# Optimization experiments

Hardware: AMD Instinct MI355X
Metric: run time of the kernel (lower is better)

Reference implementation:

```python
import jax, jax.numpy as jnp
import numpy as np
import math

B, N, C = 256, 196, 784   # n_tokens == HW == inter_dim required by the RPE matmul
HEADS = 4
HGT, WID = 14, 14
D = C // HEADS            # 196


def setup_inputs() -> dict:
    key = jax.random.key(0)
    ks = jax.random.split(key, 11)
    s = 0.02  # typical linear init scale, keeps softmax logits sane
    return {
        "x":     jax.random.normal(ks[0], (B, N, C), jnp.float32),
        "Wq":    jax.random.normal(ks[1], (C, C), jnp.float32) * s,
        "bq":    jnp.zeros((C,), jnp.float32),
        "Wk":    jax.random.normal(ks[2], (C, C), jnp.float32) * s,
        "bk":    jnp.zeros((C,), jnp.float32),
        "Wv":    jax.random.normal(ks[3], (C, C), jnp.float32) * s,
        "bv":    jnp.zeros((C,), jnp.float32),
        "Wo":    jax.random.normal(ks[4], (C, C), jnp.float32) * s,
        "bo":    jnp.zeros((C,), jnp.float32),
        "rel_h": jax.random.normal(ks[5], (1, HEADS, D, HGT, 1), jnp.float32),
        "rel_w": jax.random.normal(ks[6], (1, HEADS, D, 1, WID), jnp.float32),
    }


def reference(x, Wq, bq, Wk, bk, Wv, bv, Wo, bo, rel_h, rel_w):
    b, n, c = x.shape
    h, d = HEADS, c // HEADS

    def split_heads(t):  # (b, n, c) -> (b, h, n, d)
        return t.reshape(b, n, h, d).transpose(0, 2, 1, 3)

    q = split_heads(x @ Wq.T + bq)
    k = split_heads(x @ Wk.T + bk)
    v = split_heads(x @ Wv.T + bv)

    # (b, h, n, n) scaled dot-product scores
    sim = jnp.einsum('bhnd,bhmd->bhnm', q, k) / math.sqrt(d)

    # RPE bias: (rel_h + rel_w) -> (h, d, HW) -> (h, HW, d); matmul with q
    # treats q's token axis as the contraction axis (faithful to source).
    cp = (rel_h + rel_w).reshape(h, d, HGT * WID).transpose(0, 2, 1)  # (h, HW, d)
    pos = jnp.einsum('hpk,bhkc->bhpc', cp, q)  # (b, h, HW, d) == (b, h, n, n)

    attn = jax.nn.softmax(sim + pos, axis=-1)
    out = jnp.einsum('bhnm,bhmd->bhnd', attn, v)      # (b, h, n, d)
    out = out.transpose(0, 2, 1, 3).reshape(b, n, c)  # (b, n, c)
    return out @ Wo.T + bo
```

## Files before the change

kernel.cpp:

```cpp
#include <hip/hip_runtime.h>
#include <hip/hip_bf16.h>
#include <stdint.h>


using bf16 = __hip_bfloat16;
typedef __bf16   bf16x8 __attribute__((ext_vector_type(8)));
typedef __bf16   bf16x4 __attribute__((ext_vector_type(4)));
typedef float    f32x4  __attribute__((ext_vector_type(4)));

#define PADN 224
#define MATE (PADN*PADN)
#define MATB2 (MATE*2)
#define WROWS 896
#define KPAD 800
#define XROWB (KPAD*2)

__device__ __forceinline__ void gload16(void* lds, const void* g) {
  __builtin_amdgcn_global_load_lds(
      (const __attribute__((address_space(1))) void*)g,
      (__attribute__((address_space(3))) void*)lds, 16, 0, 0);
}

__device__ __forceinline__ void mfma_tiles(const char* bufA, const char* bufB,
                                           f32x4 (&acc)[4][4], int wr, int wc,
                                           int lane) {
  const int q = lane >> 4, c = lane & 15;
  bf16x8 a[4], b[4];
#pragma unroll
  for (int i = 0; i < 4; ++i)
    a[i] = *(const bf16x8*)(bufA + ((wr * 64 + i * 16 + c) << 6) + (q << 4));
#pragma unroll
  for (int j = 0; j < 4; ++j)
    b[j] = *(const bf16x8*)(bufB + ((wc * 64 + j * 16 + c) << 6) + (q << 4));
#pragma unroll
  for (int i = 0; i < 4; ++i)
#pragma unroll
    for (int j = 0; j < 4; ++j)
      acc[i][j] = __builtin_amdgcn_mfma_f32_16x16x32_bf16(a[i], b[j], acc[i][j], 0, 0, 0);
}

template <int EPI>
__global__ __launch_bounds__(256) void gemm_proj(
    const bf16* __restrict__ A, const bf16* __restrict__ B,
    const float* __restrict__ bias, bf16* __restrict__ d1,
    bf16* __restrict__ d2, float* __restrict__ dF, int M) {
  __shared__ __align__(16) char smem[16384];
  char* bufA = smem;
  char* bufB = smem + 8192;
  const int tid = threadIdx.x, lane = tid & 63, wave = tid >> 6;
  const int wr = wave >> 1, wc = wave & 1;
  const int m0 = blockIdx.x * 128, n0 = blockIdx.y * 128;

  f32x4 acc[4][4] = {};

  const int r0 = wave * 32 + (lane >> 2);
  const int bo = (lane & 3) << 4;
  const char* gA = (const char*)A + (size_t)(m0 + r0) * XROWB + bo;
  const char* gB = (const char*)B + (size_t)(n0 + r0) * XROWB + bo;
  char* lA = bufA + wave * 2048;
  char* lB = bufB + wave * 2048;

  for (int kc = 0; kc < 25; ++kc) {
    const int ko = kc * 64;
    gload16(lA,        gA + ko);
    gload16(lA + 1024, gA + 16 * XROWB + ko);
    gload16(lB,        gB + ko);
    gload16(lB + 1024, gB + 16 * XROWB + ko);
    __syncthreads();
    mfma_tiles(bufA, bufB, acc, wr, wc, lane);
    __syncthreads();
  }

  const int q = lane >> 4, c = lane & 15;
  if (EPI == 0 || EPI == 1) {
#pragma unroll
    for (int j = 0; j < 4; ++j) {
      const int col = n0 + wc * 64 + j * 16 + c;
      if (col >= 784) continue;
      const float bs = bias[col];
      const int hh = col / 196, dd = col - hh * 196;
#pragma unroll
      for (int i = 0; i < 4; ++i)
#pragma unroll
        for (int r = 0; r < 4; ++r) {
          const int row = m0 + wr * 64 + i * 16 + q * 4 + r;
          const int b = row / 196, n = row - b * 196;
          d1[(size_t)(b * 4 + hh) * MATE + (size_t)n * PADN + dd] =
              __float2bfloat16(acc[i][j][r] + bs);
        }
    }
  } else if (EPI == 4) {
#pragma unroll
    for (int j = 0; j < 4; ++j) {
      const int col = n0 + wc * 64 + j * 16 + c;
      if (col >= 784) continue;
      const float bs = bias[col];
#pragma unroll
      for (int i = 0; i < 4; ++i)
#pragma unroll
        for (int r = 0; r < 4; ++r) {
          const int row = m0 + wr * 64 + i * 16 + q * 4 + r;
          dF[(size_t)row * 784 + col] = acc[i][j][r] + bs;
        }
    }
  } else {
#pragma unroll
    for (int i = 0; i < 4; ++i)
#pragma unroll
      for (int r = 0; r < 4; ++r) {
        const int row = m0 + wr * 64 + i * 16 + q * 4 + r;
        if (row >= 784) continue;
        const float bs = bias[row];
        const int hh = row / 196, dd = row - hh * 196;
#pragma unroll
        for (int j = 0; j < 4; ++j) {
          const int col = n0 + wc * 64 + j * 16 + c;
          const int b = col / 196, n = col - b * 196;
          const float v = acc[i][j][r] + bs;
          const size_t o = (size_t)(b * 4 + hh) * MATE + (size_t)dd * PADN + n;
          const bf16 hv = __float2bfloat16(v);
          d1[o] = hv;
          if (EPI == 2) d2[o] = __float2bfloat16(v - __bfloat162float(hv));
        }
      }
  }
}

__global__ __launch_bounds__(256) void attn_score(
    const bf16* __restrict__ Q, const bf16* __restrict__ K,
    const bf16* __restrict__ CPh, const bf16* __restrict__ CPl,
    const bf16* __restrict__ Qth, const bf16* __restrict__ Qtl,
    float* __restrict__ S) {
  __shared__ __align__(16) char smem[24576];
  char* bufA = smem;
  char* bufB = smem + 8192;
  char* bufC = smem + 16384;
  const int tid = threadIdx.x, lane = tid & 63, wave = tid >> 6;
  const int wr = wave >> 1, wc = wave & 1;
  const int bh = blockIdx.z, h = bh & 3;
  const int m0 = blockIdx.x * 128, n0 = blockIdx.y * 128;

  f32x4 acc[4][4] = {};

  const int r0 = wave * 32 + (lane >> 2);
  const int bo = (lane & 3) << 4;
  const size_t la = (size_t)(m0 + r0) * 448 + bo;
  const size_t lb = (size_t)(n0 + r0) * 448 + bo;
  const size_t bhB = (size_t)bh * MATB2, hB = (size_t)h * MATB2;
  const char* aQ  = (const char*)Q   + bhB + la;
  const char* aK  = (const char*)K   + bhB + lb;
  const char* aCh = (const char*)CPh + hB  + la;
  const char* aCl = (const char*)CPl + hB  + la;
  const char* aTh = (const char*)Qth + bhB + lb;
  const char* aTl = (const char*)Qtl + bhB + lb;
  char* lA = bufA + wave * 2048;
  char* lB = bufB + wave * 2048;
  char* lC = bufC + wave * 2048;

  for (int kc = 0; kc < 7; ++kc) {
    const int ko = kc * 64;
    gload16(lA, aQ + ko); gload16(lA + 1024, aQ + 16 * 448 + ko);
    gload16(lB, aK + ko); gload16(lB + 1024, aK + 16 * 448 + ko);
    __syncthreads();
    mfma_tiles(bufA, bufB, acc, wr, wc, lane);
    __syncthreads();
  }
#pragma unroll
  for (int i = 0; i < 4; ++i)
#pragma unroll
    for (int j = 0; j < 4; ++j) acc[i][j] = acc[i][j] * (1.0f / 14.0f);

  for (int kc = 0; kc < 7; ++kc) {
    const int ko = kc * 64;
    gload16(lA, aCh + ko); gload16(lA + 1024, aCh + 16 * 448 + ko);
    gload16(lB, aTh + ko); gload16(lB + 1024, aTh + 16 * 448 + ko);
    gload16(lC, aTl + ko); gload16(lC + 1024, aTl + 16 * 448 + ko);
    __syncthreads();
    mfma_tiles(bufA, bufB, acc, wr, wc, lane);
    mfma_tiles(bufA, bufC, acc, wr, wc, lane);
    __syncthreads();
  }

  for (int kc = 0; kc < 7; ++kc) {
    const int ko = kc * 64;
    gload16(lA, aCl + ko); gload16(lA + 1024, aCl + 16 * 448 + ko);
    gload16(lB, aTh + ko); gload16(lB + 1024, aTh + 16 * 448 + ko);
    __syncthreads();
    mfma_tiles(bufA, bufB, acc, wr, wc, lane);
    __syncthreads();
  }

  float* Sb = S + (size_t)bh * MATE;
  const int q = lane >> 4, c = lane & 15;
#pragma unroll
  for (int i = 0; i < 4; ++i)
#pragma unroll
    for (int j = 0; j < 4; ++j)
#pragma unroll
      for (int r = 0; r < 4; ++r) {
        const int row = m0 + wr * 64 + i * 16 + q * 4 + r;
        const int col = n0 + wc * 64 + j * 16 + c;
        if (row < 196 && col < PADN) Sb[(size_t)row * PADN + col] = acc[i][j][r];
      }
}

__global__ __launch_bounds__(256) void softmax_k(const float* __restrict__ S,
                                                 bf16* __restrict__ P) {
  const int bh = blockIdx.y;
  const int row = blockIdx.x * 4 + (threadIdx.x >> 6);
  const int lane = threadIdx.x & 63;
  bf16* Pr = P + (size_t)bh * MATE + (size_t)row * PADN;
  if (row >= 196) {
#pragma unroll
    for (int k = 0; k < 4; ++k) {
      const int m = lane + k * 64;
      if (m < PADN) Pr[m] = __float2bfloat16(0.f);
    }
    return;
  }
  const float* Sr = S + (size_t)bh * MATE + (size_t)row * PADN;
  float v[4];
  float mx = -1e30f;
#pragma unroll
  for (int k = 0; k < 4; ++k) {
    const int m = lane + k * 64;
    v[k] = (m < 196) ? Sr[m] : -1e30f;
    mx = fmaxf(mx, v[k]);
  }
#pragma unroll
  for (int off = 32; off; off >>= 1) mx = fmaxf(mx, __shfl_xor(mx, off));
  float s = 0.f;
#pragma unroll
  for (int k = 0; k < 4; ++k) {
    const int m = lane + k * 64;
    v[k] = (m < 196) ? __expf(v[k] - mx) : 0.f;
    s += v[k];
  }
#pragma unroll
  for (int off = 32; off; off >>= 1) s += __shfl_xor(s, off);
  const float inv = 1.0f / s;
#pragma unroll
  for (int k = 0; k < 4; ++k) {
    const int m = lane + k * 64;
    if (m < PADN) Pr[m] = __float2bfloat16((m < 196) ? v[k] * inv : 0.f);
  }
}

__global__ __launch_bounds__(256) void attn_pv(const bf16* __restrict__ P,
                                               const bf16* __restrict__ Vt,
                                               bf16* __restrict__ O) {
  __shared__ __align__(16) char smem[16384];
  char* bufA = smem;
  char* bufB = smem + 8192;
  const int tid = threadIdx.x, lane = tid & 63, wave = tid >> 6;
  const int wr = wave >> 1, wc = wave & 1;
  const int bh = blockIdx.z;
  const int m0 = blockIdx.x * 128, n0 = blockIdx.y * 128;

  f32x4 acc[4][4] = {};

  const int r0 = wave * 32 + (lane >> 2);
  const int bo = (lane & 3) << 4;
  const size_t bhB = (size_t)bh * MATB2;
  const char* aP = (const char*)P  + bhB + (size_t)(m0 + r0) * 448 + bo;
  const char* aV = (const char*)Vt + bhB + (size_t)(n0 + r0) * 448 + bo;
  char* lA = bufA + wave * 2048;
  char* lB = bufB + wave * 2048;

  for (int kc = 0; kc < 7; ++kc) {
    const int ko = kc * 64;
    gload16(lA, aP + ko); gload16(lA + 1024, aP + 16 * 448 + ko);
    gload16(lB, aV + ko); gload16(lB + 1024, aV + 16 * 448 + ko);
    __syncthreads();
    mfma_tiles(bufA, bufB, acc, wr, wc, lane);
    __syncthreads();
  }

  const int q = lane >> 4, c = lane & 15;
  const int b = bh >> 2, h = bh & 3;
#pragma unroll
  for (int i = 0; i < 4; ++i)
#pragma unroll
    for (int j = 0; j < 4; ++j)
#pragma unroll
      for (int r = 0; r < 4; ++r) {
        const int n = m0 + wr * 64 + i * 16 + q * 4 + r;
        const int d = n0 + wc * 64 + j * 16 + c;
        if (n < 196 && d < 196)
          O[(size_t)(b * 196 + n) * KPAD + h * 196 + d] =
              __float2bfloat16(acc[i][j][r]);
      }
}

__global__ void build_cp(const float* __restrict__ rh, const float* __restrict__ rw,
                         bf16* __restrict__ CPh, bf16* __restrict__ CPl) {
  const int idx = blockIdx.x * 256 + threadIdx.x;
  if (idx >= 4 * MATE) return;
  const int h = idx / MATE;
  const int rem = idx - h * MATE;
  const int p = rem / PADN, kd = rem - (rem / PADN) * PADN;
  float v = 0.f;
  if (p < 196 && kd < 196) {
    const int gh = p / 14, gw = p - (p / 14) * 14;
    v = rh[(h * 196 + kd) * 14 + gh] + rw[(h * 196 + kd) * 14 + gw];
  }
  const bf16 hv = __float2bfloat16(v);
  CPh[idx] = hv;
  CPl[idx] = __float2bfloat16(v - __bfloat162float(hv));
}

__global__ void zero_pads(uint32_t* __restrict__ base, long nwords) {
  const long g = (long)blockIdx.x * 256 + threadIdx.x;
  if (g >= nwords) return;
  const long mat = g / 5880;
  const int w = (int)(g - mat * 5880);
  int row, off;
  if (w < 2744) { row = w / 14; off = 98 + (w - row * 14); }
  else { const int w2 = w - 2744; row = 196 + w2 / 112; off = w2 - (w2 / 112) * 112; }
  base[mat * 25088 + row * 112 + off] = 0u;
}

__global__ void zero_opad(uint32_t* __restrict__ O32, int M) {
  const int t = blockIdx.x * 256 + threadIdx.x;
  if (t >= M * 8) return;
  O32[(size_t)(t >> 3) * 400 + 392 + (t & 7)] = 0u;
}

__global__ void cvt_w_pad(const float* __restrict__ src, bf16* __restrict__ dst) {
  const int t = blockIdx.x * 256 + threadIdx.x;
  const int i = t * 4;
  const int row = i / KPAD, col = i - row * KPAD;
  f32x4 v = {0.f, 0.f, 0.f, 0.f};
  if (row < 784 && col < 784) v = *(const f32x4*)(src + (size_t)row * 784 + col);
  bf16x4 o;
  o[0] = (__bf16)v[0]; o[1] = (__bf16)v[1]; o[2] = (__bf16)v[2]; o[3] = (__bf16)v[3];
  *(bf16x4*)(dst + (size_t)row * KPAD + col) = o;
}

__global__ void cvt_x_pad(const float* __restrict__ src, bf16* __restrict__ dst,
                          int M) {
  const long t = (long)blockIdx.x * 256 + threadIdx.x;
  if (t >= (long)M * (KPAD / 4)) return;
  const long i = t * 4;
  const int row = (int)(i / KPAD), col = (int)(i - (long)row * KPAD);
  f32x4 v = {0.f, 0.f, 0.f, 0.f};
  if (col < 784) v = *(const f32x4*)(src + (size_t)row * 784 + col);
  bf16x4 o;
  o[0] = (__bf16)v[0]; o[1] = (__bf16)v[1]; o[2] = (__bf16)v[2]; o[3] = (__bf16)v[3];
  *(bf16x4*)(dst + (size_t)row * KPAD + col) = o;
}

extern "C" void kernel_launch(void* const* d_in, const int* in_sizes, int n_in,
                              void* d_out, int out_size, void* d_ws, size_t ws_size,
                              hipStream_t stream) {
  const float* x  = (const float*)d_in[0];
  const float* Wq = (const float*)d_in[1];
  const float* bq = (const float*)d_in[2];
  const float* Wk = (const float*)d_in[3];
  const float* bk = (const float*)d_in[4];
  const float* Wv = (const float*)d_in[5];
  const float* bv = (const float*)d_in[6];
  const float* Wo = (const float*)d_in[7];
  const float* bo = (const float*)d_in[8];
  const float* rh = (const float*)d_in[9];
  const float* rw = (const float*)d_in[10];
  float* out = (float*)d_out;

  const size_t MAT2B   = (size_t)MATB2;
  const size_t perBmat = 4 * MAT2B;
  const size_t perBX   = (size_t)196 * KPAD * 2;
  const size_t perBS   = 4 * (size_t)MATE * 4;
  const size_t perB    = 6 * perBmat + 2 * perBX + perBS;
  const size_t WB2     = (size_t)WROWS * KPAD * 2;
  const size_t fixed   = 4 * WB2 + 2 * perBmat + 16384;

  int CB = 256;
  while (CB > 32 && (size_t)CB * perB + fixed > ws_size) CB >>= 1;
  if ((size_t)CB * perB + fixed > ws_size) return;

  char* ws = (char*)d_ws;
  const size_t bufSz = (size_t)CB * perBmat;
  bf16*  Qb  = (bf16*)(ws);
  bf16*  Kb  = (bf16*)(ws + bufSz);
  bf16*  Qth = (bf16*)(ws + 2 * bufSz);
  bf16*  Qtl = (bf16*)(ws + 3 * bufSz);
  bf16*  Vtb = (bf16*)(ws + 4 * bufSz);
  bf16*  Pb  = (bf16*)(ws + 5 * bufSz);
  bf16*  XB  = (bf16*)(ws + 6 * bufSz);
  bf16*  Ob  = (bf16*)(ws + 6 * bufSz + (size_t)CB * perBX);
  float* S   = (float*)(ws + 6 * bufSz + (size_t)CB * 2 * perBX);
  char*  fx  = ws + 6 * bufSz + (size_t)CB * (2 * perBX + perBS);
  bf16* WqB = (bf16*)(fx);
  bf16* WkB = (bf16*)(fx + WB2);
  bf16* WvB = (bf16*)(fx + 2 * WB2);
  bf16* WoB = (bf16*)(fx + 3 * WB2);
  bf16* CPh = (bf16*)(fx + 4 * WB2);
  bf16* CPl = (bf16*)(fx + 4 * WB2 + perBmat);

  const long zw = (long)CB * 20 * 5880;
  zero_pads<<<(int)((zw + 255) / 256), 256, 0, stream>>>((uint32_t*)ws, zw);
  const int M = CB * 196;
  zero_opad<<<(M * 8 + 255) / 256, 256, 0, stream>>>((uint32_t*)Ob, M);
  build_cp<<<(4 * MATE + 255) / 256, 256, 0, stream>>>(rh, rw, CPh, CPl);
  cvt_w_pad<<<700, 256, 0, stream>>>(Wq, WqB);
  cvt_w_pad<<<700, 256, 0, stream>>>(Wk, WkB);
  cvt_w_pad<<<700, 256, 0, stream>>>(Wv, WvB);
  cvt_w_pad<<<700, 256, 0, stream>>>(Wo, WoB);

  const int gm = M / 128;
  for (int c0 = 0; c0 < 256; c0 += CB) {
    const long xt = (long)M * (KPAD / 4);
    cvt_x_pad<<<(int)((xt + 255) / 256), 256, 0, stream>>>(
        x + (size_t)c0 * 196 * 784, XB, M);

    gemm_proj<0><<<dim3(gm, 7), 256, 0, stream>>>(XB, WqB, bq, Qb, nullptr, nullptr, M);
    gemm_proj<1><<<dim3(gm, 7), 256, 0, stream>>>(XB, WkB, bk, Kb, nullptr, nullptr, M);
    gemm_proj<2><<<dim3(7, gm), 256, 0, stream>>>(WqB, XB, bq, Qth, Qtl, nullptr, M);
    gemm_proj<3><<<dim3(7, gm), 256, 0, stream>>>(WvB, XB, bv, Vtb, nullptr, nullptr, M);

    attn_score<<<dim3(2, 2, CB * 4), 256, 0, stream>>>(Qb, Kb, CPh, CPl, Qth, Qtl, S);
    softmax_k<<<dim3(56, CB * 4), 256, 0, stream>>>(S, Pb);
    attn_pv<<<dim3(2, 2, CB * 4), 256, 0, stream>>>(Pb, Vtb, Ob);

    gemm_proj<4><<<dim3(gm, 7), 256, 0, stream>>>(Ob, WoB, bo, nullptr, nullptr,
                                                  out + (size_t)c0 * 196 * 784, M);
  }
}
```

Before: 1.627 ms.

## Factor RPE bias into low-rank height/width terms and drop extra Q^T GEMM

Exploits the separable structure of rel_h + rel_w. A new kernel computes two small (14-row) projections of Q^T per batch-head, and attn_score adds them in its epilogue, replacing the 224x224x224 positional matmul that ran in split bf16 precision. The transposed hi/lo Q copies are now written from the Q projection epilogue, which removes a separate full GEMM launch. The cost is scattered transposed stores in the Q epilogue and an fp32 FMA kernel that is not on the matrix cores.

```diff
diff --git a/kernel.cpp b/kernel.cpp
--- a/kernel.cpp
+++ b/kernel.cpp
@@ -21,6 +21,12 @@
       (__attribute__((address_space(3))) void*)lds, 16, 0, 0);
 }
 
+__device__ __forceinline__ void stage2(char* lbuf, const char* g, int rowBytes,
+                                       int ko) {
+  gload16(lbuf, g + ko);
+  gload16(lbuf + 1024, g + (size_t)16 * rowBytes + ko);
+}
+
 __device__ __forceinline__ void mfma_tiles(const char* bufA, const char* bufB,
                                            f32x4 (&acc)[4][4], int wr, int wc,
                                            int lane) {
@@ -43,7 +49,8 @@
 __global__ __launch_bounds__(256) void gemm_proj(
     const bf16* __restrict__ A, const bf16* __restrict__ B,
     const float* __restrict__ bias, bf16* __restrict__ d1,
-    bf16* __restrict__ d2, float* __restrict__ dF, int M) {
+    bf16* __restrict__ d2, bf16* __restrict__ d3,
+    float* __restrict__ dF, int M) {
   __shared__ __align__(16) char smem[16384];
   char* bufA = smem;
   char* bufB = smem + 8192;
@@ -62,10 +69,8 @@
 
   for (int kc = 0; kc < 25; ++kc) {
     const int ko = kc * 64;
-    gload16(lA,        gA + ko);
-    gload16(lA + 1024, gA + 16 * XROWB + ko);
-    gload16(lB,        gB + ko);
-    gload16(lB + 1024, gB + 16 * XROWB + ko);
+    stage2(lA, gA, XROWB, ko);
+    stage2(lB, gB, XROWB, ko);
     __syncthreads();
     mfma_tiles(bufA, bufB, acc, wr, wc, lane);
     __syncthreads();
@@ -76,32 +81,41 @@
 #pragma unroll
     for (int j = 0; j < 4; ++j) {
       const int col = n0 + wc * 64 + j * 16 + c;
-      if (col >= 784) continue;
-      const float bs = bias[col];
-      const int hh = col / 196, dd = col - hh * 196;
-#pragma unroll
-      for (int i = 0; i < 4; ++i)
-#pragma unroll
-        for (int r = 0; r < 4; ++r) {
-          const int row = m0 + wr * 64 + i * 16 + q * 4 + r;
-          const int b = row / 196, n = row - b * 196;
-          d1[(size_t)(b * 4 + hh) * MATE + (size_t)n * PADN + dd] =
-              __float2bfloat16(acc[i][j][r] + bs);
-        }
+      if (col < 784) {
+        const float bs = bias[col];
+        const int hh = col / 196, dd = col - hh * 196;
+#pragma unroll
+        for (int i = 0; i < 4; ++i)
+#pragma unroll
+          for (int r = 0; r < 4; ++r) {
+            const int row = m0 + wr * 64 + i * 16 + q * 4 + r;
+            const int b = row / 196, n = row - b * 196;
+            const size_t mb = (size_t)(b * 4 + hh) * MATE;
+            const float v = acc[i][j][r] + bs;
+            const bf16 hv = __float2bfloat16(v);
+            d1[mb + (size_t)n * PADN + dd] = hv;
+            if (EPI == 0) {
+              d2[mb + (size_t)dd * PADN + n] = hv;
+              const float lo = v - __bfloat162float(hv);
+              d3[mb + (size_t)dd * PADN + n] = __float2bfloat16(lo);
+            }
+          }
+      }
     }
   } else if (EPI == 4) {
 #pragma unroll
     for (int j = 0; j < 4; ++j) {
       const int col = n0 + wc * 64 + j * 16 + c;
-      if (col >= 784) continue;
-      const float bs = bias[col];
-#pragma unroll
-      for (int i = 0; i < 4; ++i)
-#pragma unroll
-        for (int r = 0; r < 4; ++r) {
-          const int row = m0 + wr * 64 + i * 16 + q * 4 + r;
-          dF[(size_t)row * 784 + col] = acc[i][j][r] + bs;
-        }
+      if (col < 784) {
+        const float bs = bias[col];
+#pragma unroll
+        for (int i = 0; i < 4; ++i)
+#pragma unroll
+          for (int r = 0; r < 4; ++r) {
+            const int row = m0 + wr * 64 + i * 16 + q * 4 + r;
+            dF[(size_t)row * 784 + col] = acc[i][j][r] + bs;
+          }
+      }
     }
   } else {
 #pragma unroll
@@ -109,98 +123,112 @@
 #pragma unroll
       for (int r = 0; r < 4; ++r) {
         const int row = m0 + wr * 64 + i * 16 + q * 4 + r;
-        if (row >= 784) continue;
-        const float bs = bias[row];
-        const int hh = row / 196, dd = row - hh * 196;
-#pragma unroll
-        for (int j = 0; j < 4; ++j) {
-          const int col = n0 + wc * 64 + j * 16 + c;
-          const int b = col / 196, n = col - b * 196;
-          const float v = acc[i][j][r] + bs;
-          const size_t o = (size_t)(b * 4 + hh) * MATE + (size_t)dd * PADN + n;
-          const bf16 hv = __float2bfloat16(v);
-          d1[o] = hv;
-          if (EPI == 2) d2[o] = __float2bfloat16(v - __bfloat162float(hv));
+        if (row < 784) {
+          const float bs = bias[row];
+          const int hh = row / 196, dd = row - hh * 196;
+#pragma unroll
+          for (int j = 0; j < 4; ++j) {
+            const int col = n0 + wc * 64 + j * 16 + c;
+            const int b = col / 196, n = col - b * 196;
+            d1[(size_t)(b * 4 + hh) * MATE + (size_t)dd * PADN + n] =
+                __float2bfloat16(acc[i][j][r] + bs);
+          }
         }
       }
   }
+}
+
+__global__ __launch_bounds__(256) void rhw_k(
+    const float* __restrict__ rh, const float* __restrict__ rw,
+    const bf16* __restrict__ Qth, const bf16* __restrict__ Qtl,
+    float* __restrict__ RHW) {
+  __shared__ float Ts[224 * 28];
+  const int tid = threadIdx.x;
+  const int bh = blockIdx.x, h = bh & 3;
+  for (int idx = tid; idx < 224 * 28; idx += 256) {
+    const int n = idx / 28, j = idx - n * 28;
+    float v = 0.f;
+    if (n < 196)
+      v = (j < 14) ? rh[(h * 196 + n) * 14 + j]
+                   : rw[(h * 196 + n) * 14 + (j - 14)];
+    Ts[idx] = v;
+  }
+  __syncthreads();
+  const int c = tid;
+  if (c >= 224) return;
+  const char* qhB = (const char*)Qth + (size_t)bh * MATB2 + (size_t)c * 448;
+  const char* qlB = (const char*)Qtl + (size_t)bh * MATB2 + (size_t)c * 448;
+  f32x4 acc4[7] = {};
+  for (int nc = 0; nc < 28; ++nc) {
+    const bf16x8 qh = *(const bf16x8*)(qhB + nc * 16);
+    const bf16x8 ql = *(const bf16x8*)(qlB + nc * 16);
+    float qr[8];
+#pragma unroll
+    for (int e = 0; e < 8; ++e) qr[e] = (float)qh[e] + (float)ql[e];
+#pragma unroll
+    for (int e = 0; e < 8; ++e) {
+      const int n = nc * 8 + e;
+#pragma unroll
+      for (int jq = 0; jq < 7; ++jq) {
+        const f32x4 t4 = *(const f32x4*)(&Ts[n * 28 + jq * 4]);
+        acc4[jq] += t4 * qr[e];
+      }
+    }
+  }
+  float* Rb = RHW + (size_t)bh * 6272;
+#pragma unroll
+  for (int jq = 0; jq < 7; ++jq)
+#pragma unroll
+    for (int e = 0; e < 4; ++e)
+      Rb[(jq * 4 + e) * 224 + c] = acc4[jq][e];
 }
 
 __global__ __launch_bounds__(256) void attn_score(
     const bf16* __restrict__ Q, const bf16* __restrict__ K,
-    const bf16* __restrict__ CPh, const bf16* __restrict__ CPl,
-    const bf16* __restrict__ Qth, const bf16* __restrict__ Qtl,
-    float* __restrict__ S) {
-  __shared__ __align__(16) char smem[24576];
+    const float* __restrict__ RHW, float* __restrict__ S) {
+  __shared__ __align__(16) char smem[16384];
   char* bufA = smem;
   char* bufB = smem + 8192;
-  char* bufC = smem + 16384;
   const int tid = threadIdx.x, lane = tid & 63, wave = tid >> 6;
   const int wr = wave >> 1, wc = wave & 1;
-  const int bh = blockIdx.z, h = bh & 3;
+  const int bh = blockIdx.z;
   const int m0 = blockIdx.x * 128, n0 = blockIdx.y * 128;
 
   f32x4 acc[4][4] = {};
 
   const int r0 = wave * 32 + (lane >> 2);
   const int bo = (lane & 3) << 4;
-  const size_t la = (size_t)(m0 + r0) * 448 + bo;
-  const size_t lb = (size_t)(n0 + r0) * 448 + bo;
-  const size_t bhB = (size_t)bh * MATB2, hB = (size_t)h * MATB2;
-  const char* aQ  = (const char*)Q   + bhB + la;
-  const char* aK  = (const char*)K   + bhB + lb;
-  const char* aCh = (const char*)CPh + hB  + la;
-  const char* aCl = (const char*)CPl + hB  + la;
-  const char* aTh = (const char*)Qth + bhB + lb;
-  const char* aTl = (const char*)Qtl + bhB + lb;
+  const size_t bhB = (size_t)bh * MATB2;
+  const char* gA = (const char*)Q + bhB + (size_t)(m0 + r0) * 448 + bo;
+  const char* gB = (const char*)K + bhB + (size_t)(n0 + r0) * 448 + bo;
   char* lA = bufA + wave * 2048;
   char* lB = bufB + wave * 2048;
-  char* lC = bufC + wave * 2048;
 
   for (int kc = 0; kc < 7; ++kc) {
     const int ko = kc * 64;
-    gload16(lA, aQ + ko); gload16(lA + 1024, aQ + 16 * 448 + ko);
-    gload16(lB, aK + ko); gload16(lB + 1024, aK + 16 * 448 + ko);
+    stage2(lA, gA, 448, ko);
+    stage2(lB, gB, 448, ko);
     __syncthreads();
     mfma_tiles(bufA, bufB, acc, wr, wc, lane);
     __syncthreads();
   }
+
+  float* Sb = S + (size_t)bh * MATE;
+  const float* Rb = RHW + (size_t)bh * 6272;
+  const int q = lane >> 4, c = lane & 15;
 #pragma unroll
   for (int i = 0; i < 4; ++i)
 #pragma unroll
-    for (int j = 0; j < 4; ++j) acc[i][j] = acc[i][j] * (1.0f / 14.0f);
-
-  for (int kc = 0; kc < 7; ++kc) {
-    const int ko = kc * 64;
-    gload16(lA, aCh + ko); gload16(lA + 1024, aCh + 16 * 448 + ko);
-    gload16(lB, aTh + ko); gload16(lB + 1024, aTh + 16 * 448 + ko);
-    gload16(lC, aTl + ko); gload16(lC + 1024, aTl + 16 * 448 + ko);
-    __syncthreads();
-    mfma_tiles(bufA, bufB, acc, wr, wc, lane);
-    mfma_tiles(bufA, bufC, acc, wr, wc, lane);
-    __syncthreads();
-  }
-
-  for (int kc = 0; kc < 7; ++kc) {
-    const int ko = kc * 64;
-    gload16(lA, aCl + ko); gload16(lA + 1024, aCl + 16 * 448 + ko);
-    gload16(lB, aTh + ko); gload16(lB + 1024, aTh + 16 * 448 + ko);
-    __syncthreads();
-    mfma_tiles(bufA, bufB, acc, wr, wc, lane);
-    __syncthreads();
-  }
-
-  float* Sb = S + (size_t)bh * MATE;
-  const int q = lane >> 4, c = lane & 15;
-#pragma unroll
-  for (int i = 0; i < 4; ++i)
-#pragma unroll
     for (int j = 0; j < 4; ++j)
 #pragma unroll
       for (int r = 0; r < 4; ++r) {
-        const int row = m0 + wr * 64 + i * 16 + q * 4 + r;
-        const int col = n0 + wc * 64 + j * 16 + c;
-        if (row < 196 && col < PADN) Sb[(size_t)row * PADN + col] = acc[i][j][r];
+        const int p = m0 + wr * 64 + i * 16 + q * 4 + r;
+        const int cg = n0 + wc * 64 + j * 16 + c;
+        if (p < 196 && cg < 196) {
+          const int gh = p / 14, gw = p - gh * 14;
+          const float pos = Rb[gh * 224 + cg] + Rb[(14 + gw) * 224 + cg];
+          Sb[(size_t)p * PADN + cg] = acc[i][j][r] * (1.0f / 14.0f) + pos;
+        }
       }
 }
 
@@ -262,15 +290,15 @@
   const int r0 = wave * 32 + (lane >> 2);
   const int bo = (lane & 3) << 4;
   const size_t bhB = (size_t)bh * MATB2;
-  const char* aP = (const char*)P  + bhB + (size_t)(m0 + r0) * 448 + bo;
-  const char* aV = (const char*)Vt + bhB + (size_t)(n0 + r0) * 448 + bo;
+  const char* gA = (const char*)P + bhB + (size_t)(m0 + r0) * 448 + bo;
+  const char* gB = (const char*)Vt + bhB + (size_t)(n0 + r0) * 448 + bo;
   char* lA = bufA + wave * 2048;
   char* lB = bufB + wave * 2048;
 
   for (int kc = 0; kc < 7; ++kc) {
     const int ko = kc * 64;
-    gload16(lA, aP + ko); gload16(lA + 1024, aP + 16 * 448 + ko);
-    gload16(lB, aV + ko); gload16(lB + 1024, aV + 16 * 448 + ko);
+    stage2(lA, gA, 448, ko);
+    stage2(lB, gB, 448, ko);
     __syncthreads();
     mfma_tiles(bufA, bufB, acc, wr, wc, lane);
     __syncthreads();
@@ -290,23 +318,6 @@
           O[(size_t)(b * 196 + n) * KPAD + h * 196 + d] =
               __float2bfloat16(acc[i][j][r]);
       }
-}
-
-__global__ void build_cp(const float* __restrict__ rh, const float* __restrict__ rw,
-                         bf16* __restrict__ CPh, bf16* __restrict__ CPl) {
-  const int idx = blockIdx.x * 256 + threadIdx.x;
-  if (idx >= 4 * MATE) return;
-  const int h = idx / MATE;
-  const int rem = idx - h * MATE;
-  const int p = rem / PADN, kd = rem - (rem / PADN) * PADN;
-  float v = 0.f;
-  if (p < 196 && kd < 196) {
-    const int gh = p / 14, gw = p - (p / 14) * 14;
-    v = rh[(h * 196 + kd) * 14 + gh] + rw[(h * 196 + kd) * 14 + gw];
-  }
-  const bf16 hv = __float2bfloat16(v);
-  CPh[idx] = hv;
-  CPl[idx] = __float2bfloat16(v - __bfloat162float(hv));
 }
 
 __global__ void zero_pads(uint32_t* __restrict__ base, long nwords) {
@@ -366,13 +377,13 @@
   const float* rw = (const float*)d_in[10];
   float* out = (float*)d_out;
 
-  const size_t MAT2B   = (size_t)MATB2;
-  const size_t perBmat = 4 * MAT2B;
+  const size_t perBmat = 4 * (size_t)MATB2;
   const size_t perBX   = (size_t)196 * KPAD * 2;
   const size_t perBS   = 4 * (size_t)MATE * 4;
-  const size_t perB    = 6 * perBmat + 2 * perBX + perBS;
+  const size_t perBR   = 4 * (size_t)28 * 224 * 4;
+  const size_t perB    = 6 * perBmat + 2 * perBX + perBS + perBR;
   const size_t WB2     = (size_t)WROWS * KPAD * 2;
-  const size_t fixed   = 4 * WB2 + 2 * perBmat + 16384;
+  const size_t fixed   = 4 * WB2 + 16384;
 
   int CB = 256;
   while (CB > 32 && (size_t)CB * perB + fixed > ws_size) CB >>= 1;
@@ -389,19 +400,17 @@
   bf16*  XB  = (bf16*)(ws + 6 * bufSz);
   bf16*  Ob  = (bf16*)(ws + 6 * bufSz + (size_t)CB * perBX);
   float* S   = (float*)(ws + 6 * bufSz + (size_t)CB * 2 * perBX);
-  char*  fx  = ws + 6 * bufSz + (size_t)CB * (2 * perBX + perBS);
+  float* RHW = (float*)(ws + 6 * bufSz + (size_t)CB * (2 * perBX + perBS));
+  char*  fx  = ws + 6 * bufSz + (size_t)CB * (2 * perBX + perBS + perBR);
   bf16* WqB = (bf16*)(fx);
   bf16* WkB = (bf16*)(fx + WB2);
   bf16* WvB = (bf16*)(fx + 2 * WB2);
   bf16* WoB = (bf16*)(fx + 3 * WB2);
-  bf16* CPh = (bf16*)(fx + 4 * WB2);
-  bf16* CPl = (bf16*)(fx + 4 * WB2 + perBmat);
 
   const long zw = (long)CB * 20 * 5880;
   zero_pads<<<(int)((zw + 255) / 256), 256, 0, stream>>>((uint32_t*)ws, zw);
   const int M = CB * 196;
   zero_opad<<<(M * 8 + 255) / 256, 256, 0, stream>>>((uint32_t*)Ob, M);
-  build_cp<<<(4 * MATE + 255) / 256, 256, 0, stream>>>(rh, rw, CPh, CPl);
   cvt_w_pad<<<700, 256, 0, stream>>>(Wq, WqB);
   cvt_w_pad<<<700, 256, 0, stream>>>(Wk, WkB);
   cvt_w_pad<<<700, 256, 0, stream>>>(Wv, WvB);
@@ -413,16 +422,16 @@
     cvt_x_pad<<<(int)((xt + 255) / 256), 256, 0, stream>>>(
         x + (size_t)c0 * 196 * 784, XB, M);
 
-    gemm_proj<0><<<dim3(gm, 7), 256, 0, stream>>>(XB, WqB, bq, Qb, nullptr, nullptr, M);
-    gemm_proj<1><<<dim3(gm, 7), 256, 0, stream>>>(XB, WkB, bk, Kb, nullptr, nullptr, M);
-    gemm_proj<2><<<dim3(7, gm), 256, 0, stream>>>(WqB, XB, bq, Qth, Qtl, nullptr, M);
-    gemm_proj<3><<<dim3(7, gm), 256, 0, stream>>>(WvB, XB, bv, Vtb, nullptr, nullptr, M);
-
-    attn_score<<<dim3(2, 2, CB * 4), 256, 0, stream>>>(Qb, Kb, CPh, CPl, Qth, Qtl, S);
+    gemm_proj<0><<<dim3(gm, 7), 256, 0, stream>>>(XB, WqB, bq, Qb, Qth, Qtl, nullptr, M);
+    gemm_proj<1><<<dim3(gm, 7), 256, 0, stream>>>(XB, WkB, bk, Kb, nullptr, nullptr, nullptr, M);
+    gemm_proj<3><<<dim3(7, gm), 256, 0, stream>>>(WvB, XB, bv, Vtb, nullptr, nullptr, nullptr, M);
+
+    rhw_k<<<CB * 4, 256, 0, stream>>>(rh, rw, Qth, Qtl, RHW);
+    attn_score<<<dim3(2, 2, CB * 4), 256, 0, stream>>>(Qb, Kb, RHW, S);
     softmax_k<<<dim3(56, CB * 4), 256, 0, stream>>>(S, Pb);
     attn_pv<<<dim3(2, 2, CB * 4), 256, 0, stream>>>(Pb, Vtb, Ob);
 
-    gemm_proj<4><<<dim3(gm, 7), 256, 0, stream>>>(Ob, WoB, bo, nullptr, nullptr,
+    gemm_proj<4><<<dim3(gm, 7), 256, 0, stream>>>(Ob, WoB, bo, nullptr, nullptr, nullptr,
                                                   out + (size_t)c0 * 196 * 784, M);
   }
 }
```

Result: no change. 1.639 ms (+0.7%).
